# Optimization experiments

Hardware: AMD Instinct MI355X
Metric: run time of the kernel (lower is better)

The kernel has to match this reference:

```python
import jax, jax.numpy as jnp
import numpy as np

N_HEADS = 16

def setup_inputs() -> dict:
    key = jax.random.key(0)
    ks = jax.random.split(key, 5)
    B, T, C = 4, 2048, 1024
    scale = 0.02
    return {
        "x": jax.random.normal(ks[0], (B, T, C), dtype=jnp.float32),
        "w_qkv": jax.random.normal(ks[1], (C, 3 * C), dtype=jnp.float32) * scale,
        "b_qkv": jax.random.normal(ks[2], (3 * C,), dtype=jnp.float32) * scale,
        "w_out": jax.random.normal(ks[3], (C, C), dtype=jnp.float32) * scale,
        "b_out": jax.random.normal(ks[4], (C,), dtype=jnp.float32) * scale,
    }

def reference(x, w_qkv, b_qkv, w_out, b_out):
    B, T, C = x.shape
    H = N_HEADS
    D = C // H
    scale = 1.0 / jnp.sqrt(jnp.asarray(D, x.dtype))
    qkv = x @ w_qkv + b_qkv                       # (B,T,3C)
    q, k, v = jnp.split(qkv, 3, axis=-1)
    q = q.reshape(B, T, H, D).transpose(0, 2, 1, 3)  # (B,H,T,D)
    k = k.reshape(B, T, H, D).transpose(0, 2, 1, 3)
    v = v.reshape(B, T, H, D).transpose(0, 2, 1, 3)
    att = jnp.einsum("bhqd,bhkd->bhqk", q, k) * scale  # (B,H,T,T)
    causal = jnp.tril(jnp.ones((T, T), dtype=bool))
    att = jnp.where(causal[None, None], att, -jnp.inf)
    att = jax.nn.softmax(att, axis=-1)
    y = jnp.einsum("bhqk,bhkd->bhqd", att, v)     # (B,H,T,D)
    y = y.transpose(0, 2, 1, 3).reshape(B, T, C)
    return y @ w_out + b_out
```

## Files before the change

### kernel.cpp

```cpp
#include <hip/hip_runtime.h>
#include <hip/hip_bf16.h>

typedef __bf16 bf16;
typedef __attribute__((__ext_vector_type__(4))) __bf16 bf16x4;
typedef __attribute__((__ext_vector_type__(8))) __bf16 bf16x8;
typedef __attribute__((__ext_vector_type__(4))) float f32x4;

#define MFMA16(a, b, c) __builtin_amdgcn_mfma_f32_16x16x32_bf16(a, b, c, 0, 0, 0)

static __device__ __forceinline__ bf16 f2b(float f) { return (bf16)f; }

static __device__ __forceinline__ void gload16(const void* g, void* l) {
    __builtin_amdgcn_global_load_lds(
        (const __attribute__((address_space(1))) int*)g,
        (__attribute__((address_space(3))) int*)l, 16, 0, 0);
}

__global__ __launch_bounds__(256) void xcast(
    const float* __restrict__ in, bf16* __restrict__ out)
{
    size_t i = ((size_t)blockIdx.x * 256 + threadIdx.x) * 16;
    float4 a0 = *(const float4*)(in + i);
    float4 a1 = *(const float4*)(in + i + 4);
    float4 a2 = *(const float4*)(in + i + 8);
    float4 a3 = *(const float4*)(in + i + 12);
    bf16x8 p0, p1;
    p0[0] = f2b(a0.x); p0[1] = f2b(a0.y); p0[2] = f2b(a0.z); p0[3] = f2b(a0.w);
    p0[4] = f2b(a1.x); p0[5] = f2b(a1.y); p0[6] = f2b(a1.z); p0[7] = f2b(a1.w);
    p1[0] = f2b(a2.x); p1[1] = f2b(a2.y); p1[2] = f2b(a2.z); p1[3] = f2b(a2.w);
    p1[4] = f2b(a3.x); p1[5] = f2b(a3.y); p1[6] = f2b(a3.z); p1[7] = f2b(a3.w);
    *(bf16x8*)(out + i) = p0;
    *(bf16x8*)(out + i + 8) = p1;
}

__global__ __launch_bounds__(256) void cast_transpose(
    const float* __restrict__ in, bf16* __restrict__ out, int R, int Cc)
{
    __shared__ float tile[32][33];
    const int c0 = blockIdx.x * 32, r0 = blockIdx.y * 32;
    const int tx = threadIdx.x & 31, ty = threadIdx.x >> 5;
#pragma unroll
    for (int i = ty; i < 32; i += 8)
        tile[i][tx] = in[(size_t)(r0 + i) * Cc + c0 + tx];
    __syncthreads();
#pragma unroll
    for (int i = ty; i < 32; i += 8)
        out[(size_t)(c0 + i) * R + r0 + tx] = f2b(tile[tx][i]);
}

#define QSCALE (0.125f * 1.44269504f)

__global__ __launch_bounds__(256) void qkv_gemm(
    const bf16* __restrict__ Xb, const bf16* __restrict__ Wt,
    const float* __restrict__ bias,
    bf16* __restrict__ Qb, bf16* __restrict__ Kb, bf16* __restrict__ Vt)
{
    __shared__ __align__(16) bf16 As[128 * 32];
    __shared__ __align__(16) bf16 Bs[128 * 32];
    const int m0 = blockIdx.x * 128, n0 = blockIdx.y * 128;
    const int tid = threadIdx.x, lane = tid & 63, w = tid >> 6;
    const int wr = (w >> 1) * 64, wc = (w & 1) * 64;
    const int lg = lane >> 4, lr = lane & 15;
    const int srow = tid >> 2, scol = (tid & 3) * 8;
    f32x4 acc[4][4] = {};

    for (int k0 = 0; k0 < 1024; k0 += 32) {
#pragma unroll
        for (int half = 0; half < 2; ++half) {
            const int r = srow + half * 64;
            gload16(Xb + (size_t)(m0 + r) * 1024 + k0 + scol,
                    As + half * 2048 + w * 512);
            gload16(Wt + (size_t)(n0 + r) * 1024 + k0 + scol,
                    Bs + half * 2048 + w * 512);
        }
        __syncthreads();

        bf16x8 af[4], bfr[4];
#pragma unroll
        for (int m = 0; m < 4; ++m)
            af[m] = *(const bf16x8*)(As + (wr + m * 16 + lr) * 32 + lg * 8);
#pragma unroll
        for (int n = 0; n < 4; ++n)
            bfr[n] = *(const bf16x8*)(Bs + (wc + n * 16 + lr) * 32 + lg * 8);
#pragma unroll
        for (int m = 0; m < 4; ++m)
#pragma unroll
            for (int n = 0; n < 4; ++n)
                acc[m][n] = MFMA16(af[m], bfr[n], acc[m][n]);
        __syncthreads();
    }

#pragma unroll
    for (int m = 0; m < 4; ++m)
#pragma unroll
        for (int n = 0; n < 4; ++n) {
            int gn = n0 + wc + n * 16 + lr;
            int which = gn >> 10, cc = gn & 1023;
            int h = cc >> 6, d = cc & 63;
            float bv = bias[gn];
            if (which == 2) {
                int gm0 = m0 + wr + m * 16 + lg * 4;
                int b = gm0 >> 11, t0 = gm0 & 2047;
                size_t bh = (size_t)(b * 16 + h);
                bf16x4 pk;
#pragma unroll
                for (int j = 0; j < 4; ++j) pk[j] = f2b(acc[m][n][j] + bv);
                *(bf16x4*)(Vt + (bh * 64 + d) * 2048 + t0) = pk;
            } else {
#pragma unroll
                for (int j = 0; j < 4; ++j) {
                    int gm = m0 + wr + m * 16 + lg * 4 + j;
                    int b = gm >> 11, t = gm & 2047;
                    size_t bh = (size_t)(b * 16 + h);
                    if (which == 0)
                        Qb[(bh * 2048 + t) * 64 + d] =
                            f2b((acc[m][n][j] + bv) * QSCALE);
                    else
                        Kb[(bh * 2048 + t) * 64 + d] = f2b(acc[m][n][j] + bv);
                }
            }
        }
}

__global__ __launch_bounds__(256, 4) void attn(
    const bf16* __restrict__ Qb, const bf16* __restrict__ Kb,
    const bf16* __restrict__ Vt, bf16* __restrict__ Yb)
{
    __shared__ __align__(16) bf16 Ks[64 * 72];
    __shared__ __align__(16) bf16 Vs[64 * 72];
    __shared__ __align__(16) bf16 Ps[4][16 * 72];
    const int lid = blockIdx.x;
    const int xcd = lid & 7, idx = lid >> 3;
    const int bh = xcd * 8 + (idx >> 4);
    const int pair = idx & 15;
    const int ia = pair, ib = 31 - pair;
    const int q0A = ia * 64, q0B = ib * 64;
    const int tid = threadIdx.x, lane = tid & 63, w = tid >> 6;
    const int lg = lane >> 4, lr = lane & 15;

    const bf16* qrA = Qb + ((size_t)bh * 2048 + q0A + w * 16 + lr) * 64;
    bf16x8 qA0 = *(const bf16x8*)(qrA + lg * 8);
    bf16x8 qA1 = *(const bf16x8*)(qrA + 32 + lg * 8);
    const bf16* qrB = Qb + ((size_t)bh * 2048 + q0B + w * 16 + lr) * 64;
    bf16x8 qB0 = *(const bf16x8*)(qrB + lg * 8);
    bf16x8 qB1 = *(const bf16x8*)(qrB + 32 + lg * 8);

    const bf16 one = (bf16)1.0f;
    const bf16x8 vones = {one, one, one, one, one, one, one, one};

    f32x4 oA[4] = {}, oB[4] = {};
    f32x4 oLA = {}, oLB = {};

    const int sr = tid >> 2, sp = (tid & 3) * 16;

    auto sm = [&](f32x4 (&s)[4], bool diag, bf16x8& pf0, bf16x8& pf1) {
        if (diag) {
            const int qloc = w * 16 + lr;
#pragma unroll
            for (int n = 0; n < 4; ++n)
#pragma unroll
                for (int j = 0; j < 4; ++j)
                    if (n * 16 + lg * 4 + j > qloc) s[n][j] = -1e30f;
        }
#pragma unroll
        for (int n = 0; n < 4; ++n) {
            bf16x4 pk;
#pragma unroll
            for (int j = 0; j < 4; ++j)
                pk[j] = f2b(exp2f(s[n][j]));
            *(bf16x4*)(&Ps[w][lr * 72 + n * 16 + lg * 4]) = pk;
        }
        pf0 = *(const bf16x8*)(&Ps[w][lr * 72 + lg * 8]);
        pf1 = *(const bf16x8*)(&Ps[w][lr * 72 + 32 + lg * 8]);
    };

    const int ntiles = ib + 1;
    for (int it = 0; it < ntiles; ++it) {
        const int j0 = it * 64;
        const bool doA = (it <= ia);
        const bf16* ksrc = Kb + ((size_t)bh * 2048 + j0 + sr) * 64 + sp;
        *(int4*)(Ks + sr * 72 + sp)     = *(const int4*)ksrc;
        *(int4*)(Ks + sr * 72 + sp + 8) = *(const int4*)(ksrc + 8);
        const bf16* vsrc = Vt + ((size_t)bh * 64 + sr) * 2048 + j0 + sp;
        *(int4*)(Vs + sr * 72 + sp)     = *(const int4*)vsrc;
        *(int4*)(Vs + sr * 72 + sp + 8) = *(const int4*)(vsrc + 8);
        __syncthreads();

        f32x4 sA[4], sB[4];
        __builtin_amdgcn_s_setprio(1);
#pragma unroll
        for (int n = 0; n < 4; ++n) {
            bf16x8 kf0 = *(const bf16x8*)(Ks + (n * 16 + lr) * 72 + lg * 8);
            bf16x8 kf1 = *(const bf16x8*)(Ks + (n * 16 + lr) * 72 + 32 + lg * 8);
            f32x4 zb = {};
            zb = MFMA16(kf0, qB0, zb);
            zb = MFMA16(kf1, qB1, zb);
            sB[n] = zb;
            if (doA) {
                f32x4 za = {};
                za = MFMA16(kf0, qA0, za);
                za = MFMA16(kf1, qA1, za);
                sA[n] = za;
            }
        }
        __builtin_amdgcn_s_setprio(0);

        bf16x8 pfB0, pfB1, pfA0, pfA1;
        sm(sB, it == ib, pfB0, pfB1);
        if (doA) sm(sA, it == ia, pfA0, pfA1);

        __builtin_amdgcn_s_setprio(1);
        oLB = MFMA16(pfB0, vones, oLB);
        oLB = MFMA16(pfB1, vones, oLB);
        if (doA) {
            oLA = MFMA16(pfA0, vones, oLA);
            oLA = MFMA16(pfA1, vones, oLA);
        }
#pragma unroll
        for (int n = 0; n < 4; ++n) {
            bf16x8 vf0 = *(const bf16x8*)(Vs + (n * 16 + lr) * 72 + lg * 8);
            bf16x8 vf1 = *(const bf16x8*)(Vs + (n * 16 + lr) * 72 + 32 + lg * 8);
            oB[n] = MFMA16(pfB0, vf0, oB[n]);
            oB[n] = MFMA16(pfB1, vf1, oB[n]);
            if (doA) {
                oA[n] = MFMA16(pfA0, vf0, oA[n]);
                oA[n] = MFMA16(pfA1, vf1, oA[n]);
            }
        }
        __builtin_amdgcn_s_setprio(0);
        __syncthreads();
    }

    const int b = bh >> 4, h = bh & 15;
    auto wout = [&](f32x4 (&o)[4], f32x4& oL, int q0) {
        float lj[4];
#pragma unroll
        for (int j = 0; j < 4; ++j) lj[j] = 1.f / oL[j];
#pragma unroll
        for (int n = 0; n < 4; ++n)
#pragma unroll
            for (int j = 0; j < 4; ++j) {
                int qr = q0 + w * 16 + lg * 4 + j;
                Yb[((size_t)b * 2048 + qr) * 1024 + h * 64 + n * 16 + lr] =
                    f2b(o[n][j] * lj[j]);
            }
    };
    wout(oA, oLA, q0A);
    wout(oB, oLB, q0B);
}

__global__ __launch_bounds__(256) void out_gemm(
    const bf16* __restrict__ Y, const bf16* __restrict__ Wt,
    const float* __restrict__ bias, float* __restrict__ Out)
{
    __shared__ __align__(16) bf16 As[128 * 32];
    __shared__ __align__(16) bf16 Bs[128 * 32];
    const int m0 = blockIdx.x * 128, n0 = blockIdx.y * 128;
    const int tid = threadIdx.x, lane = tid & 63, w = tid >> 6;
    const int wr = (w >> 1) * 64, wc = (w & 1) * 64;
    const int lg = lane >> 4, lr = lane & 15;
    const int srow = tid >> 2, scol = (tid & 3) * 8;
    f32x4 acc[4][4] = {};

    for (int k0 = 0; k0 < 1024; k0 += 32) {
#pragma unroll
        for (int half = 0; half < 2; ++half) {
            const int r = srow + half * 64;
            gload16(Y  + (size_t)(m0 + r) * 1024 + k0 + scol,
                    As + half * 2048 + w * 512);
            gload16(Wt + (size_t)(n0 + r) * 1024 + k0 + scol,
                    Bs + half * 2048 + w * 512);
        }
        __syncthreads();

        bf16x8 af[4], bfr[4];
#pragma unroll
        for (int m = 0; m < 4; ++m)
            af[m] = *(const bf16x8*)(As + (wr + m * 16 + lr) * 32 + lg * 8);
#pragma unroll
        for (int n = 0; n < 4; ++n)
            bfr[n] = *(const bf16x8*)(Bs + (wc + n * 16 + lr) * 32 + lg * 8);
#pragma unroll
        for (int m = 0; m < 4; ++m)
#pragma unroll
            for (int n = 0; n < 4; ++n)
                acc[m][n] = MFMA16(af[m], bfr[n], acc[m][n]);
        __syncthreads();
    }

#pragma unroll
    for (int m = 0; m < 4; ++m)
#pragma unroll
        for (int n = 0; n < 4; ++n)
#pragma unroll
            for (int j = 0; j < 4; ++j) {
                int gm = m0 + wr + m * 16 + lg * 4 + j;
                int gn = n0 + wc + n * 16 + lr;
                Out[(size_t)gm * 1024 + gn] = acc[m][n][j] + bias[gn];
            }
}

extern "C" void kernel_launch(void* const* d_in, const int* in_sizes, int n_in,
                              void* d_out, int out_size, void* d_ws, size_t ws_size,
                              hipStream_t stream)
{
    const float* x     = (const float*)d_in[0];
    const float* w_qkv = (const float*)d_in[1];
    const float* b_qkv = (const float*)d_in[2];
    const float* w_out = (const float*)d_in[3];
    const float* b_out = (const float*)d_in[4];
    float* out = (float*)d_out;

    char* ws = (char*)d_ws;
    bf16* wqkvT = (bf16*)(ws);
    bf16* woutT = (bf16*)(ws + 6291456);
    bf16* Qb    = (bf16*)(ws + 6291456 + 2097152);
    bf16* Kb    = (bf16*)(ws + 6291456 + 2097152 + 16777216);
    bf16* Vt    = (bf16*)(ws + 6291456 + 2097152 + 2u * 16777216u);
    bf16* Xb    = (bf16*)(ws + 6291456 + 2097152 + 3u * 16777216u);
    bf16* Yb    = Xb;

    xcast<<<2048, 256, 0, stream>>>(x, Xb);
    cast_transpose<<<dim3(96, 32), 256, 0, stream>>>(w_qkv, wqkvT, 1024, 3072);
    cast_transpose<<<dim3(32, 32), 256, 0, stream>>>(w_out, woutT, 1024, 1024);
    qkv_gemm<<<dim3(64, 24), 256, 0, stream>>>(Xb, wqkvT, b_qkv, Qb, Kb, Vt);
    attn<<<1024, 256, 0, stream>>>(Qb, Kb, Vt, Yb);
    out_gemm<<<dim3(64, 8), 256, 0, stream>>>(Yb, woutT, b_out, out);
}
```

Measured before the change: 175.4 us.

## Double-buffer K/V tiles in attention with register prefetch and XOR-swizzled LDS

The attention loop now prefetches the next K/V tile into registers at the start of each iteration and writes it into the other of two LDS buffers after compute. This drops one barrier per iteration and overlaps global-load latency with the MFMA work. The padded 72-stride LDS layout is replaced by a 64-stride XOR swizzle for K, V and P to avoid bank conflicts without padding. In exchange, LDS usage roughly doubles for K/V and register pressure rises, which may reduce occupancy under launch_bounds(256,4).

```diff
diff --git a/kernel.cpp b/kernel.cpp
--- a/kernel.cpp
+++ b/kernel.cpp
@@ -126,9 +126,9 @@
     const bf16* __restrict__ Qb, const bf16* __restrict__ Kb,
     const bf16* __restrict__ Vt, bf16* __restrict__ Yb)
 {
-    __shared__ __align__(16) bf16 Ks[64 * 72];
-    __shared__ __align__(16) bf16 Vs[64 * 72];
-    __shared__ __align__(16) bf16 Ps[4][16 * 72];
+    __shared__ __align__(16) bf16 Ks[2 * 64 * 64];
+    __shared__ __align__(16) bf16 Vs[2 * 64 * 64];
+    __shared__ __align__(16) bf16 Ps[4][16 * 64];
     const int lid = blockIdx.x;
     const int xcd = lid & 7, idx = lid >> 3;
     const int bh = xcd * 8 + (idx >> 4);
@@ -151,7 +151,33 @@
     f32x4 oA[4] = {}, oB[4] = {};
     f32x4 oLA = {}, oLB = {};
 
-    const int sr = tid >> 2, sp = (tid & 3) * 16;
+    const int sr = tid >> 2;
+    const int c0 = (tid & 3) * 2;
+    const int sp = c0 * 8;
+    const int d0 = sr * 64 + ((c0 ^ (sr & 7)) << 3);
+    const int d1 = sr * 64 + (((c0 + 1) ^ (sr & 7)) << 3);
+    const int swa = ((lg ^ (lr & 7)) << 3);
+    const int swb = (((lg + 4) ^ (lr & 7)) << 3);
+    const int pbase = lr * 64 + (lg & 1) * 4;
+
+    int4 kst0, kst1, vst0, vst1;
+    auto issue = [&](int it) {
+        const int j0 = it * 64;
+        const bf16* ksrc = Kb + ((size_t)bh * 2048 + j0 + sr) * 64 + sp;
+        kst0 = *(const int4*)ksrc;
+        kst1 = *(const int4*)(ksrc + 8);
+        const bf16* vsrc = Vt + ((size_t)bh * 64 + sr) * 2048 + j0 + sp;
+        vst0 = *(const int4*)vsrc;
+        vst1 = *(const int4*)(vsrc + 8);
+    };
+    auto commit = [&](int b) {
+        bf16* Kd = Ks + b * 4096;
+        bf16* Vd = Vs + b * 4096;
+        *(int4*)(Kd + d0) = kst0;
+        *(int4*)(Kd + d1) = kst1;
+        *(int4*)(Vd + d0) = vst0;
+        *(int4*)(Vd + d1) = vst1;
+    };
 
     auto sm = [&](f32x4 (&s)[4], bool diag, bf16x8& pf0, bf16x8& pf1) {
         if (diag) {
@@ -168,30 +194,31 @@
 #pragma unroll
             for (int j = 0; j < 4; ++j)
                 pk[j] = f2b(exp2f(s[n][j]));
-            *(bf16x4*)(&Ps[w][lr * 72 + n * 16 + lg * 4]) = pk;
-        }
-        pf0 = *(const bf16x8*)(&Ps[w][lr * 72 + lg * 8]);
-        pf1 = *(const bf16x8*)(&Ps[w][lr * 72 + 32 + lg * 8]);
+            *(bf16x4*)(&Ps[w][pbase + (((n * 2 + (lg >> 1)) ^ (lr & 7)) << 3)]) = pk;
+        }
+        pf0 = *(const bf16x8*)(&Ps[w][lr * 64 + swa]);
+        pf1 = *(const bf16x8*)(&Ps[w][lr * 64 + swb]);
     };
 
     const int ntiles = ib + 1;
+    issue(0);
+    commit(0);
+    __syncthreads();
+
     for (int it = 0; it < ntiles; ++it) {
-        const int j0 = it * 64;
         const bool doA = (it <= ia);
-        const bf16* ksrc = Kb + ((size_t)bh * 2048 + j0 + sr) * 64 + sp;
-        *(int4*)(Ks + sr * 72 + sp)     = *(const int4*)ksrc;
-        *(int4*)(Ks + sr * 72 + sp + 8) = *(const int4*)(ksrc + 8);
-        const bf16* vsrc = Vt + ((size_t)bh * 64 + sr) * 2048 + j0 + sp;
-        *(int4*)(Vs + sr * 72 + sp)     = *(const int4*)vsrc;
-        *(int4*)(Vs + sr * 72 + sp + 8) = *(const int4*)(vsrc + 8);
-        __syncthreads();
+        const bool more = (it + 1 < ntiles);
+        if (more) issue(it + 1);
+        const bf16* Kr = Ks + (it & 1) * 4096;
+        const bf16* Vr = Vs + (it & 1) * 4096;
 
         f32x4 sA[4], sB[4];
         __builtin_amdgcn_s_setprio(1);
 #pragma unroll
         for (int n = 0; n < 4; ++n) {
-            bf16x8 kf0 = *(const bf16x8*)(Ks + (n * 16 + lr) * 72 + lg * 8);
-            bf16x8 kf1 = *(const bf16x8*)(Ks + (n * 16 + lr) * 72 + 32 + lg * 8);
+            const bf16* krow = Kr + (n * 16 + lr) * 64;
+            bf16x8 kf0 = *(const bf16x8*)(krow + swa);
+            bf16x8 kf1 = *(const bf16x8*)(krow + swb);
             f32x4 zb = {};
             zb = MFMA16(kf0, qB0, zb);
             zb = MFMA16(kf1, qB1, zb);
@@ -218,8 +245,9 @@
         }
 #pragma unroll
         for (int n = 0; n < 4; ++n) {
-            bf16x8 vf0 = *(const bf16x8*)(Vs + (n * 16 + lr) * 72 + lg * 8);
-            bf16x8 vf1 = *(const bf16x8*)(Vs + (n * 16 + lr) * 72 + 32 + lg * 8);
+            const bf16* vrow = Vr + (n * 16 + lr) * 64;
+            bf16x8 vf0 = *(const bf16x8*)(vrow + swa);
+            bf16x8 vf1 = *(const bf16x8*)(vrow + swb);
             oB[n] = MFMA16(pfB0, vf0, oB[n]);
             oB[n] = MFMA16(pfB1, vf1, oB[n]);
             if (doA) {
@@ -228,6 +256,8 @@
             }
         }
         __builtin_amdgcn_s_setprio(0);
+
+        if (more) commit((it + 1) & 1);
         __syncthreads();
     }
 
```

Measured after the change: 249.4 us. 42.2% more time.
